# Performance work log

Hardware: AMD Instinct MI355X
Metric: run time of the kernel (lower is better)

## Reference

```python
import jax, jax.numpy as jnp
import numpy as np

NEG_SLOPE = 0.01  # torch LeakyReLU default

def leaky_relu(x):
    return jnp.where(x >= 0, x, NEG_SLOPE * x)

def gcn_conv(x, W, b, row, col, num_nodes):
    # PyG GCNConv: add self-loops, symmetric normalization, then X W aggregation.
    h = x @ W  # [N, H]
    loops = jnp.arange(num_nodes, dtype=row.dtype)
    r = jnp.concatenate([row, loops])
    c = jnp.concatenate([col, loops])
    ones = jnp.ones(r.shape[0], dtype=x.dtype)
    deg = jax.ops.segment_sum(ones, c, num_segments=num_nodes)  # in-degree with self-loops
    dinv = jnp.where(deg > 0, jax.lax.rsqrt(deg), 0.0)
    norm = dinv[r] * dinv[c]  # [E+N]
    msg = h[r] * norm[:, None]  # gather-transform, [E+N, H]
    out = jax.ops.segment_sum(msg, c, num_segments=num_nodes)  # scatter-add
    return out + b

def global_mean_pool(x, batch, num_graphs):
    s = jax.ops.segment_sum(x, batch, num_segments=num_graphs)
    cnt = jax.ops.segment_sum(jnp.ones(x.shape[0], dtype=x.dtype), batch, num_segments=num_graphs)
    return s / jnp.maximum(cnt, 1.0)[:, None]

def setup_inputs() -> dict:
    N, E, G = 100000, 1600000, 256
    IN, H, GF, OUT = 64, 128, 32, 1
    key = jax.random.key(0)
    ks = jax.random.split(key, 16)
    inp = {}
    inp["x"] = jax.random.normal(ks[0], (N, IN), dtype=jnp.float32)
    inp["edge_index"] = jax.random.randint(ks[1], (2, E), 0, N, dtype=jnp.int64)
    inp["batch"] = jnp.sort(jax.random.randint(ks[2], (N,), 0, G, dtype=jnp.int64))
    inp["graph_feature"] = jax.random.normal(ks[3], (G, GF), dtype=jnp.float32)
    def lin(k, fan_in, fan_out):
        kw, kb = jax.random.split(k)
        bound = 1.0 / np.sqrt(fan_in)
        W = jax.random.uniform(kw, (fan_in, fan_out), jnp.float32, -bound, bound)
        b = jax.random.uniform(kb, (fan_out,), jnp.float32, -bound, bound)
        return W, b
    inp["W1"], inp["b1"] = lin(ks[4], IN, H)
    inp["W2"], inp["b2"] = lin(ks[5], H, H)
    inp["Wg"], inp["bg"] = lin(ks[6], H, H)      # gnn_proj
    inp["Wf"], inp["bf"] = lin(ks[7], GF, H)     # graph_feature_proj
    inp["Wm1"], inp["bm1"] = lin(ks[8], 2 * H, H)  # fusion linear 1
    inp["Wm2"], inp["bm2"] = lin(ks[9], H, OUT)    # fusion linear 2
    return inp

def reference(x, edge_index, batch, graph_feature, W1, b1, W2, b2, Wg, bg, Wf, bf, Wm1, bm1, Wm2, bm2):
    N = x.shape[0]
    G = graph_feature.shape[0]
    row, col = edge_index[0], edge_index[1]
    h = leaky_relu(gcn_conv(x, W1, b1, row, col, N))
    h = leaky_relu(gcn_conv(h, W2, b2, row, col, N))
    pooled = global_mean_pool(h, batch, G)          # [G, H]
    gnn_feat = pooled @ Wg + bg
    graph_feat = graph_feature @ Wf + bf
    fused = jnp.concatenate([gnn_feat, graph_feat], axis=1)  # [G, 2H]
    z = leaky_relu(fused)
    z = leaky_relu(z @ Wm1 + bm1)
    return z @ Wm2 + bm2
```

## Files before the change

### kernel.cpp

```cpp
#include <hip/hip_runtime.h>
#include <hip/hip_fp16.h>

#define CBW  1024
#define CBSH 10
#define CCAP 20480
#define SRCM 0x1FFFF

typedef _Float16 f16x8 __attribute__((ext_vector_type(8)));
typedef float f32x4 __attribute__((ext_vector_type(4)));

__device__ __forceinline__ float lrelu(float v) { return v >= 0.0f ? v : 0.01f * v; }

__global__ __launch_bounds__(256) void k_part(const int* __restrict__ row,
                                              const int* __restrict__ col,
                                              int* __restrict__ bcur,
                                              unsigned* __restrict__ bedges, int E, int NB) {
  __shared__ int hist[128];
  __shared__ int gbase[128];
  const int t = threadIdx.x;
  const int base = blockIdx.x * 2048 + t * 8;
  int r[8], c[8];
  if (base + 8 <= E) {
    int4 r0 = *(const int4*)&row[base], r1 = *(const int4*)&row[base + 4];
    int4 c0 = *(const int4*)&col[base], c1 = *(const int4*)&col[base + 4];
    r[0] = r0.x; r[1] = r0.y; r[2] = r0.z; r[3] = r0.w;
    r[4] = r1.x; r[5] = r1.y; r[6] = r1.z; r[7] = r1.w;
    c[0] = c0.x; c[1] = c0.y; c[2] = c0.z; c[3] = c0.w;
    c[4] = c1.x; c[5] = c1.y; c[6] = c1.z; c[7] = c1.w;
  } else {
#pragma unroll
    for (int j = 0; j < 8; ++j) {
      bool ok = (base + j) < E;
      r[j] = ok ? row[base + j] : 0;
      c[j] = ok ? col[base + j] : -1;
    }
  }
  if (t < 128) hist[t] = 0;
  __syncthreads();
#pragma unroll
  for (int j = 0; j < 8; ++j)
    if (c[j] >= 0) atomicAdd(&hist[c[j] >> CBSH], 1);
  __syncthreads();
  if (t < NB && hist[t] > 0) gbase[t] = atomicAdd(&bcur[t * 16], hist[t]);
  __syncthreads();
  if (t < 128) hist[t] = 0;
  __syncthreads();
#pragma unroll
  for (int j = 0; j < 8; ++j) {
    if (c[j] < 0) continue;
    int b = c[j] >> CBSH;
    int lp = atomicAdd(&hist[b], 1);
    int p = gbase[b] + lp;
    if (p < CCAP)
      bedges[(size_t)b * CCAP + p] = ((unsigned)(c[j] & (CBW - 1)) << 17) | (unsigned)r[j];
  }
}

__global__ __launch_bounds__(256) void k_csr(const int* __restrict__ bcur,
                                             const unsigned* __restrict__ bedges,
                                             int* __restrict__ rowstart,
                                             float* __restrict__ dinv,
                                             unsigned* __restrict__ csr, int N, int NB) {
  __shared__ int hist[CBW];
  __shared__ int tsum[256];
  __shared__ int bpre[128];
  int b = blockIdx.x, t = threadIdx.x;
  if (t < 128) bpre[t] = (t < NB) ? min(bcur[t * 16], CCAP) : 0;
  for (int i = t; i < CBW; i += 256) hist[i] = 0;
  __syncthreads();
  for (int off = 1; off < 128; off <<= 1) {
    int x = (t < 128 && t >= off) ? bpre[t - off] : 0;
    __syncthreads();
    if (t < 128) bpre[t] += x;
    __syncthreads();
  }
  const int gbs = (b > 0) ? bpre[b - 1] : 0;
  const int cnt = min(bcur[b * 16], CCAP);
  const unsigned* be = bedges + (size_t)b * CCAP;
  for (int i = t; i < cnt; i += 256) atomicAdd(&hist[be[i] >> 17], 1);
  __syncthreads();
  int h0 = hist[t * 4], h1 = hist[t * 4 + 1], h2 = hist[t * 4 + 2], h3 = hist[t * 4 + 3];
  int s0 = h0, s1 = s0 + h1, s2 = s1 + h2, s3 = s2 + h3;
  tsum[t] = s3;
  __syncthreads();
  for (int off = 1; off < 256; off <<= 1) {
    int x = (t >= off) ? tsum[t - off] : 0;
    __syncthreads();
    tsum[t] += x;
    __syncthreads();
  }
  int prefix = (t > 0) ? tsum[t - 1] : 0;
  int node0 = (b << CBSH) + t * 4;
  int ends[4] = {s0, s1, s2, s3};
  int hs[4] = {h0, h1, h2, h3};
#pragma unroll
  for (int j = 0; j < 4; ++j) {
    int node = node0 + j;
    if (node < N) {
      rowstart[node + 1] = gbs + prefix + ends[j];
      dinv[node] = rsqrtf((float)hs[j] + 1.0f);
    }
  }
  if (b == 0 && t == 0) rowstart[0] = 0;
  __syncthreads();
#pragma unroll
  for (int j = 0; j < 4; ++j) hist[t * 4 + j] = gbs + prefix + ends[j] - hs[j];
  __syncthreads();
  for (int i = t; i < cnt; i += 256) {
    unsigned pe = be[i];
    int pos = atomicAdd(&hist[pe >> 17], 1);
    csr[pos] = pe & SRCM;
  }
}

__device__ __forceinline__ void cvtW_one(const float* W, __half* Wf, int idx) {
  int i = idx & 7, l = (idx >> 3) & 63, cb = (idx >> 9) & 7, kc = idx >> 12;
  int ks = kc * 32 + ((l >> 4) << 3) + i;
  int c = cb * 16 + (l & 15);
  Wf[idx] = __float2half(W[ks * 128 + c]);
}
__global__ __launch_bounds__(256) void k_cvt(const float* __restrict__ X,
                                             const float* __restrict__ dinv,
                                             __half* __restrict__ Xs, int nxblk, size_t total4,
                                             const float* __restrict__ W1,
                                             const float* __restrict__ W2,
                                             __half* __restrict__ Wf1,
                                             __half* __restrict__ Wf2) {
  int blk = blockIdx.x;
  if (blk < nxblk) {
    size_t i = (size_t)blk * 256 + threadIdx.x;
    if (i >= total4) return;
    float d = dinv[i >> 4];
    float4 v = *(const float4*)&X[i * 4];
    __half2* dst = (__half2*)&Xs[i * 4];
    dst[0] = __floats2half2_rn(v.x * d, v.y * d);
    dst[1] = __floats2half2_rn(v.z * d, v.w * d);
  } else {
    int idx = (blk - nxblk) * 256 + threadIdx.x;
    if (idx < 64 * 128) cvtW_one(W1, Wf1, idx);
    else if (idx < 192 * 128) cvtW_one(W2, Wf2, idx - 64 * 128);
  }
}

__global__ __launch_bounds__(256) void k_agg64s(const int* __restrict__ rowstart,
                                                const unsigned* __restrict__ csr,
                                                const __half* __restrict__ Xs,
                                                __half* __restrict__ O, int N) {
  int wid = (blockIdx.x * 256 + threadIdx.x) >> 6;
  int lane = threadIdx.x & 63;
  if (wid >= N) return;
  int s = rowstart[wid], e = rowstart[wid + 1];
  float acc = __half2float(Xs[(size_t)wid * 64 + lane]);
#pragma unroll 4
  for (int i = s; i < e; ++i)
    acc += __half2float(Xs[(size_t)csr[i] * 64 + lane]);
  O[(size_t)wid * 64 + lane] = __float2half(acc);
}

__global__ __launch_bounds__(256) void k_agg128s(const int* __restrict__ rowstart,
                                                 const unsigned* __restrict__ csr,
                                                 const __half* __restrict__ H,
                                                 __half* __restrict__ O, int N) {
  int wid = (blockIdx.x * 256 + threadIdx.x) >> 6;
  int lane = threadIdx.x & 63;
  if (wid >= N) return;
  int s = rowstart[wid], e = rowstart[wid + 1];
  const __half2* Hv = (const __half2*)H;
  float2 acc = __half22float2(Hv[(size_t)wid * 64 + lane]);
#pragma unroll 4
  for (int i = s; i < e; ++i) {
    float2 h = __half22float2(Hv[(size_t)csr[i] * 64 + lane]);
    acc.x += h.x;
    acc.y += h.y;
  }
  ((__half2*)O)[(size_t)wid * 64 + lane] = __floats2half2_rn(acc.x, acc.y);
}

__global__ __launch_bounds__(256) void k_gemm1(const __half* __restrict__ A,
                                               const __half* __restrict__ Wf,
                                               const float* __restrict__ bias,
                                               const float* __restrict__ dinv,
                                               __half* __restrict__ Y, int N) {
  const int t = threadIdx.x;
  const int l = t & 63;
  const int lr = l & 15, lg = l >> 4;
  const int rowbase = blockIdx.x * 64 + (t >> 6) * 16;
  if (rowbase >= N) return;
  f32x4 acc[8];
#pragma unroll
  for (int cb = 0; cb < 8; ++cb) acc[cb] = (f32x4){0.f, 0.f, 0.f, 0.f};
  int arow = min(rowbase + lr, N - 1);
  const _Float16* Ap = (const _Float16*)A + (size_t)arow * 64 + lg * 8;
  const _Float16* Wp = (const _Float16*)Wf + (size_t)l * 8;
#pragma unroll
  for (int kc = 0; kc < 2; ++kc) {
    f16x8 a = *(const f16x8*)(Ap + kc * 32);
#pragma unroll
    for (int cb = 0; cb < 8; ++cb) {
      f16x8 b = *(const f16x8*)(Wp + (size_t)((kc * 8 + cb) * 64) * 8);
      acc[cb] = __builtin_amdgcn_mfma_f32_16x16x32_f16(a, b, acc[cb], 0, 0, 0);
    }
  }
  float d[4];
#pragma unroll
  for (int v = 0; v < 4; ++v) {
    int gr = rowbase + lg * 4 + v;
    d[v] = (gr < N) ? dinv[gr] : 0.f;
  }
#pragma unroll
  for (int cb = 0; cb < 8; ++cb) {
    int c = cb * 16 + lr;
    float bv = bias[c];
#pragma unroll
    for (int v = 0; v < 4; ++v) {
      int gr = rowbase + lg * 4 + v;
      if (gr < N)
        Y[(size_t)gr * 128 + c] = __float2half(lrelu(acc[cb][v] * d[v] + bv) * d[v]);
    }
  }
}

__global__ __launch_bounds__(256) void k_gemm2pool(const __half* __restrict__ A,
                                                   const __half* __restrict__ Wf,
                                                   const float* __restrict__ bias,
                                                   const float* __restrict__ dinv,
                                                   const int* __restrict__ batch,
                                                   float* __restrict__ pooled, int N) {
  const int t = threadIdx.x;
  const int l = t & 63;
  const int lr = l & 15, lg = l >> 4;
  const int rowbase = blockIdx.x * 64 + (t >> 6) * 16;
  if (rowbase >= N) return;
  f32x4 acc[8];
#pragma unroll
  for (int cb = 0; cb < 8; ++cb) acc[cb] = (f32x4){0.f, 0.f, 0.f, 0.f};
  int arow = min(rowbase + lr, N - 1);
  const _Float16* Ap = (const _Float16*)A + (size_t)arow * 128 + lg * 8;
  const _Float16* Wp = (const _Float16*)Wf + (size_t)l * 8;
#pragma unroll
  for (int kc = 0; kc < 4; ++kc) {
    f16x8 a = *(const f16x8*)(Ap + kc * 32);
#pragma unroll
    for (int cb = 0; cb < 8; ++cb) {
      f16x8 b = *(const f16x8*)(Wp + (size_t)((kc * 8 + cb) * 64) * 8);
      acc[cb] = __builtin_amdgcn_mfma_f32_16x16x32_f16(a, b, acc[cb], 0, 0, 0);
    }
  }
  float d[4];
#pragma unroll
  for (int v = 0; v < 4; ++v) {
    int gr = rowbase + lg * 4 + v;
    d[v] = (gr < N) ? dinv[gr] : 0.f;
  }
  int glo = batch[rowbase];
  int ghi = batch[min(rowbase + 15, N - 1)];
  if (glo == ghi) {
#pragma unroll
    for (int cb = 0; cb < 8; ++cb) {
      int c = cb * 16 + lr;
      float bv = bias[c];
      float s = 0.f;
#pragma unroll
      for (int v = 0; v < 4; ++v) {
        int gr = rowbase + lg * 4 + v;
        if (gr < N) s += lrelu(acc[cb][v] * d[v] + bv);
      }
      s += __shfl_xor(s, 16);
      s += __shfl_xor(s, 32);
      if (lg == 0) atomicAdd(&pooled[(size_t)glo * 128 + c], s);
    }
  } else {
#pragma unroll
    for (int cb = 0; cb < 8; ++cb) {
      int c = cb * 16 + lr;
      float bv = bias[c];
#pragma unroll
      for (int v = 0; v < 4; ++v) {
        int gr = rowbase + lg * 4 + v;
        if (gr < N)
          atomicAdd(&pooled[(size_t)batch[gr] * 128 + c], lrelu(acc[cb][v] * d[v] + bv));
      }
    }
  }
}

__global__ __launch_bounds__(128) void k_head(const float* __restrict__ pooled,
                                              const int* __restrict__ batch, int N,
                                              const float* __restrict__ gfeat,
                                              const float* __restrict__ Wg, const float* __restrict__ bg,
                                              const float* __restrict__ Wf, const float* __restrict__ bf,
                                              const float* __restrict__ Wm1, const float* __restrict__ bm1,
                                              const float* __restrict__ Wm2, const float* __restrict__ bm2,
                                              float* __restrict__ out) {
  __shared__ float p[128], a[256], qf[32], red[2];
  __shared__ int se[2];
  int g = blockIdx.x, t = threadIdx.x;
  if (t < 2) {
    int target = g + t;
    int lo = 0, hi = N;
    while (lo < hi) {
      int mid = (lo + hi) >> 1;
      if (batch[mid] < target) lo = mid + 1; else hi = mid;
    }
    se[t] = lo;
  }
  if (t >= 2 && t < 34) qf[t - 2] = gfeat[(size_t)g * 32 + (t - 2)];
  __syncthreads();
  float inv = 1.0f / fmaxf((float)(se[1] - se[0]), 1.0f);
  p[t] = pooled[(size_t)g * 128 + t] * inv;
  __syncthreads();
  float z1 = bg[t];
  for (int m = 0; m < 128; ++m) z1 += p[m] * Wg[m * 128 + t];
  float z2 = bf[t];
  for (int m = 0; m < 32; ++m) z2 += qf[m] * Wf[m * 128 + t];
  a[t] = lrelu(z1);
  a[128 + t] = lrelu(z2);
  __syncthreads();
  float z = bm1[t];
  for (int k = 0; k < 256; ++k) z += a[k] * Wm1[k * 128 + t];
  z = lrelu(z);
  float v = z * Wm2[t];
#pragma unroll
  for (int off = 32; off; off >>= 1) v += __shfl_down(v, off);
  if ((t & 63) == 0) red[t >> 6] = v;
  __syncthreads();
  if (t == 0) out[g] = red[0] + red[1] + bm2[0];
}

extern "C" void kernel_launch(void* const* d_in, const int* in_sizes, int n_in,
                              void* d_out, int out_size, void* d_ws, size_t ws_size,
                              hipStream_t stream) {
  const float* x     = (const float*)d_in[0];
  const int*   ei    = (const int*)d_in[1];
  const int*   batch = (const int*)d_in[2];
  const float* gfeat = (const float*)d_in[3];
  const float* W1 = (const float*)d_in[4];
  const float* b1 = (const float*)d_in[5];
  const float* W2 = (const float*)d_in[6];
  const float* b2 = (const float*)d_in[7];
  const float* Wg = (const float*)d_in[8];
  const float* bg = (const float*)d_in[9];
  const float* Wf = (const float*)d_in[10];
  const float* bf = (const float*)d_in[11];
  const float* Wm1 = (const float*)d_in[12];
  const float* bm1 = (const float*)d_in[13];
  const float* Wm2 = (const float*)d_in[14];
  const float* bm2 = (const float*)d_in[15];
  float* out = (float*)d_out;

  const int N = in_sizes[0] / 64;
  const int E = in_sizes[1] / 2;
  const int G = in_sizes[3] / 32;
  const int* row = ei;
  const int* col = ei + E;
  const int NB = (N + CBW - 1) >> CBSH;

  char* w = (char*)d_ws;
  size_t off = 0;
  auto alloc = [&](size_t bytes) {
    void* p = w + off;
    off = (off + bytes + 255) & ~(size_t)255;
    return p;
  };
  int*      bcur     = (int*)alloc((size_t)NB * 16 * 4);
  float*    pooled   = (float*)alloc((size_t)G * 128 * 4);
  size_t    zspan    = off;
  int*      rowstart = (int*)alloc((size_t)(N + 1) * 4);
  float*    dinv     = (float*)alloc((size_t)N * 4);
  __half*   Wf1      = (__half*)alloc((size_t)64 * 128 * 2);
  __half*   Wf2      = (__half*)alloc((size_t)128 * 128 * 2);
  unsigned* csr      = (unsigned*)alloc((size_t)E * 4);
  __half*   Xs       = (__half*)alloc((size_t)N * 64 * 2);
  __half*   h1s      = (__half*)alloc((size_t)N * 128 * 2);
  char*     regionB  = (char*)alloc((size_t)N * 128 * 2);
  unsigned* bedges   = (unsigned*)regionB;
  __half*   S2       = (__half*)regionB;
  __half*   S64      = (__half*)alloc((size_t)N * 64 * 2);
  (void)ws_size;

  hipMemsetAsync(bcur, 0, zspan, stream);

  k_part<<<(E + 2047) / 2048, 256, 0, stream>>>(row, col, bcur, bedges, E, NB);
  k_csr<<<NB, 256, 0, stream>>>(bcur, bedges, rowstart, dinv, csr, N, NB);

  const size_t total4 = (size_t)N * 16;
  const int nxblk = (int)((total4 + 255) / 256);
  k_cvt<<<nxblk + 96, 256, 0, stream>>>(x, dinv, Xs, nxblk, total4, W1, W2, Wf1, Wf2);

  const int aggGrid = (N * 64 + 255) / 256;
  const int gemmGrid = (N + 63) / 64;

  k_agg64s<<<aggGrid, 256, 0, stream>>>(rowstart, csr, Xs, S64, N);
  k_gemm1<<<gemmGrid, 256, 0, stream>>>(S64, Wf1, b1, dinv, h1s, N);

  k_agg128s<<<aggGrid, 256, 0, stream>>>(rowstart, csr, h1s, S2, N);
  k_gemm2pool<<<gemmGrid, 256, 0, stream>>>(S2, Wf2, b2, dinv, batch, pooled, N);

  k_head<<<G, 128, 0, stream>>>(pooled, batch, N, gfeat, Wg, bg, Wf, bf, Wm1, bm1, Wm2, bm2, out);
}
```

Measured before the change: 275.6 us.

## Store gathered node features in FP8 and split edge loops across lane slots

Input features and first-layer activations are now stored as packed FP8 (e4m3-style) instead of fp16, halving the bytes each random gather pulls during both aggregation passes. The aggregation kernels give each lane four packed values, split a node's edge list across 4 or 2 lane slots, and combine the partial sums with cross-lane shuffles. Because the first GEMM now writes each row's values in a permuted column order, W2 is permuted to match. This trades accuracy, since FP8 has far less mantissa and range than fp16, for less gather bandwidth, and adds encode/decode work.

```diff
diff --git a/kernel.cpp b/kernel.cpp
--- a/kernel.cpp
+++ b/kernel.cpp
@@ -8,8 +8,64 @@
 
 typedef _Float16 f16x8 __attribute__((ext_vector_type(8)));
 typedef float f32x4 __attribute__((ext_vector_type(4)));
+typedef float f32x2 __attribute__((ext_vector_type(2)));
 
 __device__ __forceinline__ float lrelu(float v) { return v >= 0.0f ? v : 0.01f * v; }
+
+#if __has_builtin(__builtin_amdgcn_cvt_pk_f32_fp8) && __has_builtin(__builtin_amdgcn_cvt_pk_fp8_f32)
+#define FP8_HW 1
+#else
+#define FP8_HW 0
+#endif
+
+#if !FP8_HW
+__device__ __forceinline__ float dec1(unsigned b) {
+  unsigned s = b & 0x80, e = (b >> 3) & 15, m = b & 7;
+  float v = e ? __uint_as_float(((e + 120u) << 23) | (m << 20))
+              : (float)m * 0.001953125f;
+  return s ? -v : v;
+}
+__device__ __forceinline__ unsigned enc1(float v) {
+  unsigned h = __half_as_ushort(__float2half_rn(v));
+  unsigned s = (h >> 8) & 0x80;
+  int e = (h >> 10) & 31;
+  unsigned m = h & 1023;
+  if (e == 0) return s;
+  if (e > 23) return s | 0x7E;
+  if (e < 9) {
+    float a = fabsf(v) * 512.0f;
+    unsigned M = (unsigned)(a + 0.5f);
+    if (M > 7) return s | 0x08;
+    return s | M;
+  }
+  unsigned m3 = m >> 7, rest = m & 127;
+  if (rest > 64 || (rest == 64 && (m3 & 1))) {
+    if (++m3 == 8) { m3 = 0; if (++e > 23) return s | 0x7E; }
+  }
+  return s | ((unsigned)(e - 8) << 3) | m3;
+}
+#endif
+
+__device__ __forceinline__ void dec4(unsigned q, float& a, float& b, float& c, float& d) {
+#if FP8_HW
+  f32x2 lo = __builtin_amdgcn_cvt_pk_f32_fp8((int)q, false);
+  f32x2 hi = __builtin_amdgcn_cvt_pk_f32_fp8((int)q, true);
+  a = lo[0]; b = lo[1]; c = hi[0]; d = hi[1];
+#else
+  a = dec1(q & 255); b = dec1((q >> 8) & 255);
+  c = dec1((q >> 16) & 255); d = dec1(q >> 24);
+#endif
+}
+
+__device__ __forceinline__ unsigned enc4(float a, float b, float c, float d) {
+#if FP8_HW
+  int r = __builtin_amdgcn_cvt_pk_fp8_f32(a, b, 0, false);
+  r = __builtin_amdgcn_cvt_pk_fp8_f32(c, d, r, true);
+  return (unsigned)r;
+#else
+  return enc1(a) | (enc1(b) << 8) | (enc1(c) << 16) | (enc1(d) << 24);
+#endif
+}
 
 __global__ __launch_bounds__(256) void k_part(const int* __restrict__ row,
                                               const int* __restrict__ col,
@@ -113,15 +169,16 @@
   }
 }
 
-__device__ __forceinline__ void cvtW_one(const float* W, __half* Wf, int idx) {
+__device__ __forceinline__ void cvtW_one(const float* W, __half* Wf, int idx, bool perm) {
   int i = idx & 7, l = (idx >> 3) & 63, cb = (idx >> 9) & 7, kc = idx >> 12;
   int ks = kc * 32 + ((l >> 4) << 3) + i;
+  if (perm) ks = (ks & 7) * 16 + (ks >> 3);
   int c = cb * 16 + (l & 15);
   Wf[idx] = __float2half(W[ks * 128 + c]);
 }
 __global__ __launch_bounds__(256) void k_cvt(const float* __restrict__ X,
                                              const float* __restrict__ dinv,
-                                             __half* __restrict__ Xs, int nxblk, size_t total4,
+                                             unsigned* __restrict__ X8, int nxblk, size_t total4,
                                              const float* __restrict__ W1,
                                              const float* __restrict__ W2,
                                              __half* __restrict__ Wf1,
@@ -132,55 +189,79 @@
     if (i >= total4) return;
     float d = dinv[i >> 4];
     float4 v = *(const float4*)&X[i * 4];
-    __half2* dst = (__half2*)&Xs[i * 4];
-    dst[0] = __floats2half2_rn(v.x * d, v.y * d);
-    dst[1] = __floats2half2_rn(v.z * d, v.w * d);
+    X8[i] = enc4(v.x * d, v.y * d, v.z * d, v.w * d);
   } else {
     int idx = (blk - nxblk) * 256 + threadIdx.x;
-    if (idx < 64 * 128) cvtW_one(W1, Wf1, idx);
-    else if (idx < 192 * 128) cvtW_one(W2, Wf2, idx - 64 * 128);
-  }
-}
-
-__global__ __launch_bounds__(256) void k_agg64s(const int* __restrict__ rowstart,
+    if (idx < 64 * 128) cvtW_one(W1, Wf1, idx, false);
+    else if (idx < 192 * 128) cvtW_one(W2, Wf2, idx - 64 * 128, true);
+  }
+}
+
+__global__ __launch_bounds__(256) void k_agg64q(const int* __restrict__ rowstart,
                                                 const unsigned* __restrict__ csr,
-                                                const __half* __restrict__ Xs,
+                                                const unsigned* __restrict__ X8,
                                                 __half* __restrict__ O, int N) {
   int wid = (blockIdx.x * 256 + threadIdx.x) >> 6;
   int lane = threadIdx.x & 63;
   if (wid >= N) return;
+  int qd = lane & 15, slot = lane >> 4;
   int s = rowstart[wid], e = rowstart[wid + 1];
-  float acc = __half2float(Xs[(size_t)wid * 64 + lane]);
-#pragma unroll 4
-  for (int i = s; i < e; ++i)
-    acc += __half2float(Xs[(size_t)csr[i] * 64 + lane]);
-  O[(size_t)wid * 64 + lane] = __float2half(acc);
-}
-
-__global__ __launch_bounds__(256) void k_agg128s(const int* __restrict__ rowstart,
+  float ax = 0.f, ay = 0.f, az = 0.f, aw = 0.f;
+  if (slot == 0) dec4(X8[(size_t)wid * 16 + qd], ax, ay, az, aw);
+#pragma unroll 2
+  for (int i = s + slot; i < e; i += 4) {
+    unsigned src = csr[i];
+    float bx, by, bz, bw;
+    dec4(X8[(size_t)src * 16 + qd], bx, by, bz, bw);
+    ax += bx; ay += by; az += bz; aw += bw;
+  }
+  ax += __shfl_xor(ax, 16); ay += __shfl_xor(ay, 16);
+  az += __shfl_xor(az, 16); aw += __shfl_xor(aw, 16);
+  ax += __shfl_xor(ax, 32); ay += __shfl_xor(ay, 32);
+  az += __shfl_xor(az, 32); aw += __shfl_xor(aw, 32);
+  if (slot == 0) {
+    __half2 h0 = __floats2half2_rn(ax, ay), h1 = __floats2half2_rn(az, aw);
+    uint2 st;
+    st.x = *(unsigned*)&h0;
+    st.y = *(unsigned*)&h1;
+    *(uint2*)(O + (size_t)wid * 64 + qd * 4) = st;
+  }
+}
+
+__global__ __launch_bounds__(256) void k_agg128q(const int* __restrict__ rowstart,
                                                  const unsigned* __restrict__ csr,
-                                                 const __half* __restrict__ H,
+                                                 const unsigned* __restrict__ H8,
                                                  __half* __restrict__ O, int N) {
   int wid = (blockIdx.x * 256 + threadIdx.x) >> 6;
   int lane = threadIdx.x & 63;
   if (wid >= N) return;
+  int qd = lane & 31, slot = lane >> 5;
   int s = rowstart[wid], e = rowstart[wid + 1];
-  const __half2* Hv = (const __half2*)H;
-  float2 acc = __half22float2(Hv[(size_t)wid * 64 + lane]);
-#pragma unroll 4
-  for (int i = s; i < e; ++i) {
-    float2 h = __half22float2(Hv[(size_t)csr[i] * 64 + lane]);
-    acc.x += h.x;
-    acc.y += h.y;
-  }
-  ((__half2*)O)[(size_t)wid * 64 + lane] = __floats2half2_rn(acc.x, acc.y);
+  float ax = 0.f, ay = 0.f, az = 0.f, aw = 0.f;
+  if (slot == 0) dec4(H8[(size_t)wid * 32 + qd], ax, ay, az, aw);
+#pragma unroll 2
+  for (int i = s + slot; i < e; i += 2) {
+    unsigned src = csr[i];
+    float bx, by, bz, bw;
+    dec4(H8[(size_t)src * 32 + qd], bx, by, bz, bw);
+    ax += bx; ay += by; az += bz; aw += bw;
+  }
+  ax += __shfl_xor(ax, 32); ay += __shfl_xor(ay, 32);
+  az += __shfl_xor(az, 32); aw += __shfl_xor(aw, 32);
+  if (slot == 0) {
+    __half2 h0 = __floats2half2_rn(ax, ay), h1 = __floats2half2_rn(az, aw);
+    uint2 st;
+    st.x = *(unsigned*)&h0;
+    st.y = *(unsigned*)&h1;
+    *(uint2*)(O + (size_t)wid * 128 + qd * 4) = st;
+  }
 }
 
 __global__ __launch_bounds__(256) void k_gemm1(const __half* __restrict__ A,
                                                const __half* __restrict__ Wf,
                                                const float* __restrict__ bias,
                                                const float* __restrict__ dinv,
-                                               __half* __restrict__ Y, int N) {
+                                               unsigned char* __restrict__ H8, int N) {
   const int t = threadIdx.x;
   const int l = t & 63;
   const int lr = l & 15, lg = l >> 4;
@@ -201,22 +282,19 @@
       acc[cb] = __builtin_amdgcn_mfma_f32_16x16x32_f16(a, b, acc[cb], 0, 0, 0);
     }
   }
-  float d[4];
 #pragma unroll
   for (int v = 0; v < 4; ++v) {
     int gr = rowbase + lg * 4 + v;
-    d[v] = (gr < N) ? dinv[gr] : 0.f;
-  }
-#pragma unroll
-  for (int cb = 0; cb < 8; ++cb) {
-    int c = cb * 16 + lr;
-    float bv = bias[c];
-#pragma unroll
-    for (int v = 0; v < 4; ++v) {
-      int gr = rowbase + lg * 4 + v;
-      if (gr < N)
-        Y[(size_t)gr * 128 + c] = __float2half(lrelu(acc[cb][v] * d[v] + bv) * d[v]);
-    }
+    if (gr >= N) continue;
+    float d = dinv[gr];
+    float y[8];
+#pragma unroll
+    for (int cb = 0; cb < 8; ++cb)
+      y[cb] = lrelu(acc[cb][v] * d + bias[cb * 16 + lr]) * d;
+    uint2 st;
+    st.x = enc4(y[0], y[1], y[2], y[3]);
+    st.y = enc4(y[4], y[5], y[6], y[7]);
+    *(uint2*)(H8 + (size_t)gr * 128 + lr * 8) = st;
   }
 }
 
@@ -370,12 +448,12 @@
   __half*   Wf1      = (__half*)alloc((size_t)64 * 128 * 2);
   __half*   Wf2      = (__half*)alloc((size_t)128 * 128 * 2);
   unsigned* csr      = (unsigned*)alloc((size_t)E * 4);
-  __half*   Xs       = (__half*)alloc((size_t)N * 64 * 2);
-  __half*   h1s      = (__half*)alloc((size_t)N * 128 * 2);
+  unsigned* x8       = (unsigned*)alloc((size_t)N * 64);
+  unsigned char* h18 = (unsigned char*)alloc((size_t)N * 128);
+  __half*   S64      = (__half*)alloc((size_t)N * 64 * 2);
   char*     regionB  = (char*)alloc((size_t)N * 128 * 2);
   unsigned* bedges   = (unsigned*)regionB;
   __half*   S2       = (__half*)regionB;
-  __half*   S64      = (__half*)alloc((size_t)N * 64 * 2);
   (void)ws_size;
 
   hipMemsetAsync(bcur, 0, zspan, stream);
@@ -385,15 +463,15 @@
 
   const size_t total4 = (size_t)N * 16;
   const int nxblk = (int)((total4 + 255) / 256);
-  k_cvt<<<nxblk + 96, 256, 0, stream>>>(x, dinv, Xs, nxblk, total4, W1, W2, Wf1, Wf2);
+  k_cvt<<<nxblk + 96, 256, 0, stream>>>(x, dinv, x8, nxblk, total4, W1, W2, Wf1, Wf2);
 
   const int aggGrid = (N * 64 + 255) / 256;
   const int gemmGrid = (N + 63) / 64;
 
-  k_agg64s<<<aggGrid, 256, 0, stream>>>(rowstart, csr, Xs, S64, N);
-  k_gemm1<<<gemmGrid, 256, 0, stream>>>(S64, Wf1, b1, dinv, h1s, N);
-
-  k_agg128s<<<aggGrid, 256, 0, stream>>>(rowstart, csr, h1s, S2, N);
+  k_agg64q<<<aggGrid, 256, 0, stream>>>(rowstart, csr, x8, S64, N);
+  k_gemm1<<<gemmGrid, 256, 0, stream>>>(S64, Wf1, b1, dinv, h18, N);
+
+  k_agg128q<<<aggGrid, 256, 0, stream>>>(rowstart, csr, (const unsigned*)h18, S2, N);
   k_gemm2pool<<<gemmGrid, 256, 0, stream>>>(S2, Wf2, b2, dinv, batch, pooled, N);
 
   k_head<<<G, 128, 0, stream>>>(pooled, batch, N, gfeat, Wg, bg, Wf, bf, Wm1, bm1, Wm2, bm2, out);
```

Measured after the change: 253.5 us. 8.0% less time.
